# Performance work log

Hardware: AMD Instinct MI355X
Metric: run time of the kernel (lower is better)

Reference implementation:

```python
import jax, jax.numpy as jnp
import numpy as np

T, B, D, H, DEPTH = 256, 64, 1024, 1024, 2


def setup_inputs() -> dict:
    key = jax.random.key(0)
    ks = jax.random.split(key, 12)
    s_in = (1.0 / (D + H)) ** 0.5  # torch Linear default init scale
    s_h = (1.0 / H) ** 0.5
    qc_v = jax.random.uniform(ks[9], (DEPTH, H, H), jnp.float32, -s_h, s_h)
    # weight_norm init: g = ||v|| per output row, so initial w == v
    qc_g = jnp.linalg.norm(qc_v, axis=2)
    return {
        "inputs": jax.random.normal(ks[0], (T, B, D), jnp.float32),
        "Wf": jax.random.uniform(ks[1], (H, D + H), jnp.float32, -s_in, s_in),
        "bf": jax.random.uniform(ks[2], (H,), jnp.float32, -s_in, s_in),
        "Wi": jax.random.uniform(ks[3], (H, D + H), jnp.float32, -s_in, s_in),
        "bi": jax.random.uniform(ks[4], (H,), jnp.float32, -s_in, s_in),
        "Wu": jax.random.uniform(ks[5], (H, D + H), jnp.float32, -s_in, s_in),
        "bu": jax.random.uniform(ks[6], (H,), jnp.float32, -s_in, s_in),
        "Wo": jax.random.uniform(ks[7], (H, D + H), jnp.float32, -s_in, s_in),
        "bo": jax.random.uniform(ks[8], (H,), jnp.float32, -s_in, s_in),
        "qc_v": qc_v,
        "qc_g": qc_g,
        "qc_b": jax.random.uniform(ks[10], (DEPTH, H), jnp.float32, -s_h, s_h),
    }


def reference(inputs, Wf, bf, Wi, bi, Wu, bu, Wo, bo, qc_v, qc_g, qc_b):
    # weight_norm (dim=0): w = g * v / ||v||_row
    qc_w = qc_g[:, :, None] * qc_v / jnp.linalg.norm(qc_v, axis=2, keepdims=True)

    def qc(x):  # x: [4, B, H] -> tanh(linear) applied DEPTH times (shared across gates)
        for d in range(DEPTH):
            x = jnp.tanh(jnp.einsum('gbh,oh->gbo', x, qc_w[d]) + qc_b[d])
        return x

    h0 = jnp.zeros((inputs.shape[1], bf.shape[0]), inputs.dtype)

    def step(carry, x):
        hx, cx = carry
        comb = jnp.concatenate([x, hx], axis=1)  # [B, D+H]
        f = jax.nn.sigmoid(comb @ Wf.T + bf)
        i = jax.nn.sigmoid(comb @ Wi.T + bi)
        g = jnp.tanh(comb @ Wu.T + bu)
        o = jax.nn.sigmoid(comb @ Wo.T + bo)
        f, i, g, o = qc(jnp.stack([f, i, g, o]))
        cx = f * cx + i * g
        hx = o * jnp.tanh(cx)
        return (hx, cx), hx

    (hx, cx), outputs = jax.lax.scan(step, (h0, h0), inputs)
    return outputs, hx, cx
```

## Files before the change

kernel.cpp:

```cpp
#include <hip/hip_runtime.h>
#include <cstdint>
#include <cstddef>

typedef float f32x4 __attribute__((ext_vector_type(4)));
typedef __bf16 bf16x8 __attribute__((ext_vector_type(8)));

#define T_STEPS 256
#define HD      1024
#define DHK     2048

__device__ __forceinline__ unsigned short f2bf(float f) {
  union { float f; unsigned u; } v; v.f = f;
  unsigned r = v.u + 0x7fffu + ((v.u >> 16) & 1u);
  return (unsigned short)(r >> 16);
}

__device__ __forceinline__ float fast_sigmoid(float x) {
  return 1.0f / (1.0f + __expf(-x));
}
__device__ __forceinline__ float fast_tanh(float x) {
  float e = __expf(2.0f * x);
  return (e - 1.0f) / (e + 1.0f);
}

__device__ __forceinline__ f32x4 mfma16(bf16x8 a, bf16x8 b, f32x4 c) {
  return __builtin_amdgcn_mfma_f32_16x16x32_bf16(a, b, c, 0, 0, 0);
}

#define LOADC(dst, vofs, base, IMM)                                            \
  asm volatile("global_load_dwordx4 %0, %1, %2 offset:" IMM " sc0 sc1"         \
               : "=v"(dst) : "v"(vofs), "s"(base) : "memory")

#define L8(st, vofs, base)                                                     \
  LOADC(st[0], vofs, base, "0");   LOADC(st[1], vofs, base, "64");             \
  LOADC(st[2], vofs, base, "128"); LOADC(st[3], vofs, base, "192");            \
  LOADC(st[4], vofs, base, "256"); LOADC(st[5], vofs, base, "320");            \
  LOADC(st[6], vofs, base, "384"); LOADC(st[7], vofs, base, "448")

#define WAITV0()                                                               \
  do { asm volatile("s_waitcnt vmcnt(0)" ::: "memory");                        \
       __builtin_amdgcn_sched_barrier(0); } while (0)

#define MF8(st, w, accv)                                                       \
  accv = mfma16(st[0], (w)[0], accv); accv = mfma16(st[1], (w)[1], accv);      \
  accv = mfma16(st[2], (w)[2], accv); accv = mfma16(st[3], (w)[3], accv);      \
  accv = mfma16(st[4], (w)[4], accv); accv = mfma16(st[5], (w)[5], accv);      \
  accv = mfma16(st[6], (w)[6], accv); accv = mfma16(st[7], (w)[7], accv)

__device__ __forceinline__ void storec8(void* p, ushort4 v) {
  asm volatile("global_store_dwordx2 %0, %1, off sc0 sc1"
               :: "v"(p), "v"(v) : "memory");
}
__device__ __forceinline__ void storec2(void* p, unsigned short v) {
  unsigned vv = v;
  asm volatile("global_store_short %0, %1, off sc0 sc1"
               :: "v"(p), "v"(vv) : "memory");
}

__device__ __forceinline__ void release_flag(int* f, int v) {
  asm volatile("s_waitcnt vmcnt(0)" ::: "memory");
  __hip_atomic_store(f, v, __ATOMIC_RELAXED, __HIP_MEMORY_SCOPE_AGENT);
}
__device__ __forceinline__ void wait_ge(const int* f, int v) {
  while (__hip_atomic_load(f, __ATOMIC_RELAXED, __HIP_MEMORY_SCOPE_AGENT) < v)
    __builtin_amdgcn_s_sleep(2);
  asm volatile("" ::: "memory");
}

__global__ __launch_bounds__(256, 1) void qlstm_persist(
    const unsigned short* __restrict__ Xbf,
    const unsigned short* __restrict__ Wbf,
    const unsigned short* __restrict__ qcw,
    const float* __restrict__ bias_cat,
    const float* __restrict__ qcb,
    unsigned short* __restrict__ Gbf,
    unsigned short* __restrict__ G2bf,
    unsigned short* __restrict__ hbf,
    float* __restrict__ c_state,
    float* __restrict__ out,
    int* __restrict__ aA, int* __restrict__ aB, int* __restrict__ aC) {
  const int nb = blockIdx.x, tid = threadIdx.x;
  const int wv = tid >> 6, lane = tid & 63;
  const int l15 = lane & 15, l16 = lane >> 4;
  const int q = nb >> 6;
  const int n0 = (nb & 63) * 16;
  const int kb = wv * 256;

  __shared__ __align__(16) float red[4][16][68];

  bf16x8 wA[16], wB[8], wC[8];
  {
    const unsigned short* wrow = Wbf + (size_t)(nb * 16 + l15) * DHK;
#pragma unroll
    for (int s = 0; s < 8; ++s)
      wA[s] = *(const bf16x8*)&wrow[kb + s * 32 + l16 * 8];
#pragma unroll
    for (int s = 0; s < 8; ++s)
      wA[8 + s] = *(const bf16x8*)&wrow[1024 + kb + s * 32 + l16 * 8];
    const unsigned short* qrow0 = qcw + (size_t)(n0 + l15) * HD;
    const unsigned short* qrow1 = qrow0 + (size_t)HD * HD;
#pragma unroll
    for (int s = 0; s < 8; ++s) {
      wB[s] = *(const bf16x8*)&qrow0[kb + s * 32 + l16 * 8];
      wC[s] = *(const bf16x8*)&qrow1[kb + s * 32 + l16 * 8];
    }
  }
  const f32x4 biasA = *(const f32x4*)&bias_cat[nb * 16 + (tid & 3) * 4];
  const f32x4 biasB = *(const f32x4*)&qcb[n0 + (tid & 3) * 4];
  const float biasC = qcb[HD + n0 + (tid & 15)];

  const int erow = tid >> 2, ecb = (tid & 3) * 4;
  const int bl = tid >> 4, cc = tid & 15;

  int vofsAB[4], vofsC[4];
#pragma unroll
  for (int mt = 0; mt < 4; ++mt) {
    vofsAB[mt] = (((mt * 16 + l15) * HD) + kb + l16 * 8) * 2;
    vofsC[mt]  = (((mt * 64 + q * 16 + l15) * HD) + kb + l16 * 8) * 2;
  }
  const unsigned short* hB  = hbf;
  const unsigned short* gB  = Gbf + (size_t)(q * 64) * HD;
  const unsigned short* g2B = G2bf;

  for (int t = 0; t < T_STEPS; ++t) {
    {
      f32x4 acc[4] = {};
      const unsigned short* xb = Xbf + (size_t)t * (64 * HD);
#pragma unroll
      for (int s = 0; s < 8; ++s) {
        const int k = kb + s * 32 + l16 * 8;
#pragma unroll
        for (int mt = 0; mt < 4; ++mt) {
          bf16x8 a = *(const bf16x8*)&xb[(size_t)(mt * 16 + l15) * HD + k];
          acc[mt] = mfma16(a, wA[s], acc[mt]);
        }
      }
      wait_ge(&aC[tid], t);
      __syncthreads();
      {
        bf16x8 s0[8], s1[8], s2[8], s3[8];
        L8(s0, vofsAB[0], hB); L8(s1, vofsAB[1], hB);
        L8(s2, vofsAB[2], hB); L8(s3, vofsAB[3], hB);
        WAITV0();
        MF8(s0, wA + 8, acc[0]); MF8(s1, wA + 8, acc[1]);
        MF8(s2, wA + 8, acc[2]); MF8(s3, wA + 8, acc[3]);
      }
#pragma unroll
      for (int mt = 0; mt < 4; ++mt)
        *(f32x4*)&red[wv][l15][mt * 16 + l16 * 4] = acc[mt];
      __syncthreads();
      ushort4 pk;
#pragma unroll
      for (int i = 0; i < 4; ++i) {
        float v = red[0][ecb + i][erow] + red[1][ecb + i][erow] +
                  red[2][ecb + i][erow] + red[3][ecb + i][erow] + biasA[i];
        v = (q == 2) ? fast_tanh(v) : fast_sigmoid(v);
        ((unsigned short*)&pk)[i] = f2bf(v);
      }
      storec8(&Gbf[(size_t)(q * 64 + erow) * HD + n0 + ecb], pk);
      __syncthreads();
      if (tid == 0) release_flag(&aA[nb], t + 1);
    }
    {
      if (tid < 64) wait_ge(&aA[q * 64 + tid], t + 1);
      __syncthreads();
      f32x4 acc[4] = {};
      {
        bf16x8 s0[8], s1[8], s2[8], s3[8];
        L8(s0, vofsAB[0], gB); L8(s1, vofsAB[1], gB);
        L8(s2, vofsAB[2], gB); L8(s3, vofsAB[3], gB);
        WAITV0();
        MF8(s0, wB, acc[0]); MF8(s1, wB, acc[1]);
        MF8(s2, wB, acc[2]); MF8(s3, wB, acc[3]);
      }
#pragma unroll
      for (int mt = 0; mt < 4; ++mt)
        *(f32x4*)&red[wv][l15][mt * 16 + l16 * 4] = acc[mt];
      __syncthreads();
      ushort4 pk;
#pragma unroll
      for (int i = 0; i < 4; ++i) {
        float v = red[0][ecb + i][erow] + red[1][ecb + i][erow] +
                  red[2][ecb + i][erow] + red[3][ecb + i][erow] + biasB[i];
        ((unsigned short*)&pk)[i] = f2bf(fast_tanh(v));
      }
      storec8(&G2bf[(size_t)(q * 64 + erow) * HD + n0 + ecb], pk);
      __syncthreads();
      if (tid == 0) release_flag(&aB[nb], t + 1);
    }
    {
      wait_ge(&aB[tid], t + 1);
      __syncthreads();
      f32x4 acc[4] = {};
      {
        bf16x8 s0[8], s1[8], s2[8], s3[8];
        L8(s0, vofsC[0], g2B); L8(s1, vofsC[1], g2B);
        L8(s2, vofsC[2], g2B); L8(s3, vofsC[3], g2B);
        WAITV0();
        MF8(s0, wC, acc[0]); MF8(s1, wC, acc[1]);
        MF8(s2, wC, acc[2]); MF8(s3, wC, acc[3]);
      }
#pragma unroll
      for (int mt = 0; mt < 4; ++mt)
        *(f32x4*)&red[wv][l15][mt * 16 + l16 * 4] = acc[mt];
      __syncthreads();
      float gv[4];
#pragma unroll
      for (int g = 0; g < 4; ++g) {
        float v = red[0][cc][g * 16 + bl] + red[1][cc][g * 16 + bl] +
                  red[2][cc][g * 16 + bl] + red[3][cc][g * 16 + bl] + biasC;
        gv[g] = fast_tanh(v);
      }
      const int ci = (q * 16 + bl) * HD + n0 + cc;
      const float c_new = gv[0] * c_state[ci] + gv[1] * gv[2];
      const float h_new = gv[3] * fast_tanh(c_new);
      c_state[ci] = c_new;
      out[(size_t)t * (64 * HD) + ci] = h_new;
      storec2(&hbf[ci], f2bf(h_new));
      if (t == T_STEPS - 1) {
        out[(size_t)T_STEPS * (64 * HD) + ci] = h_new;
        out[(size_t)T_STEPS * (64 * HD) + 64 * HD + ci] = c_new;
      }
      __syncthreads();
      if (tid == 0) release_flag(&aC[nb], t + 1);
    }
  }
}

__global__ void xconv_kernel(const float* __restrict__ x,
                             unsigned short* __restrict__ xbf, int n4) {
  int idx = blockIdx.x * blockDim.x + threadIdx.x;
  int stride = gridDim.x * blockDim.x;
  for (int i = idx; i < n4; i += stride) {
    float4 v = ((const float4*)x)[i];
    ushort4 o;
    o.x = f2bf(v.x); o.y = f2bf(v.y); o.z = f2bf(v.z); o.w = f2bf(v.w);
    ((ushort4*)xbf)[i] = o;
  }
}

__global__ void wconv_kernel(const float* __restrict__ Wf, const float* __restrict__ Wi,
                             const float* __restrict__ Wu, const float* __restrict__ Wo,
                             const float* __restrict__ bfv, const float* __restrict__ biv,
                             const float* __restrict__ buv, const float* __restrict__ bov,
                             unsigned short* __restrict__ Wbf, float* __restrict__ bias_cat) {
  const int n = blockIdx.x;
  const int gate = n >> 10, r = n & 1023;
  const float* W = gate == 0 ? Wf : gate == 1 ? Wi : gate == 2 ? Wu : Wo;
  const float* src = W + (size_t)r * DHK;
  unsigned short* dst = Wbf + (size_t)n * DHK;
  for (int k = threadIdx.x; k < DHK; k += 256) dst[k] = f2bf(src[k]);
  if (threadIdx.x == 0) {
    const float* bsrc = gate == 0 ? bfv : gate == 1 ? biv : gate == 2 ? buv : bov;
    bias_cat[n] = bsrc[r];
  }
}

__global__ void qcw_kernel(const float* __restrict__ qcv, const float* __restrict__ qcg,
                           unsigned short* __restrict__ qcw) {
  const int row = blockIdx.x * 4 + (threadIdx.x >> 6);
  const int lane = threadIdx.x & 63;
  const float* v = qcv + (size_t)row * HD;
  float ss = 0.0f;
#pragma unroll
  for (int j = 0; j < 16; ++j) { float a = v[j * 64 + lane]; ss += a * a; }
#pragma unroll
  for (int off = 32; off > 0; off >>= 1) ss += __shfl_xor(ss, off);
  const float scale = qcg[row] / sqrtf(ss);
#pragma unroll
  for (int j = 0; j < 16; ++j)
    qcw[(size_t)row * HD + j * 64 + lane] = f2bf(v[j * 64 + lane] * scale);
}

__global__ void init_state_kernel(unsigned short* __restrict__ hbf,
                                  float* __restrict__ c_state,
                                  int* __restrict__ flags) {
  int i = blockIdx.x * blockDim.x + threadIdx.x;
  hbf[i] = 0;
  c_state[i] = 0.0f;
  if (i < 768) flags[i] = 0;
}

extern "C" void kernel_launch(void* const* d_in, const int* in_sizes, int n_in,
                              void* d_out, int out_size, void* d_ws, size_t ws_size,
                              hipStream_t stream) {
  const float* x   = (const float*)d_in[0];
  const float* Wf  = (const float*)d_in[1];
  const float* bfv = (const float*)d_in[2];
  const float* Wi  = (const float*)d_in[3];
  const float* biv = (const float*)d_in[4];
  const float* Wu  = (const float*)d_in[5];
  const float* buv = (const float*)d_in[6];
  const float* Wo  = (const float*)d_in[7];
  const float* bov = (const float*)d_in[8];
  const float* qcv = (const float*)d_in[9];
  const float* qcg = (const float*)d_in[10];
  const float* qcb = (const float*)d_in[11];
  float* out = (float*)d_out;

  char* p = (char*)d_ws;
  auto alloc = [&](size_t bytes) {
    char* r = p; p += (bytes + 255) & ~(size_t)255; return r;
  };
  unsigned short* Xbf  = (unsigned short*)alloc((size_t)T_STEPS * 64 * HD * 2);
  unsigned short* Wbf  = (unsigned short*)alloc((size_t)4096 * DHK * 2);
  unsigned short* qcw  = (unsigned short*)alloc((size_t)2 * HD * HD * 2);
  float* bias_cat      = (float*)alloc((size_t)4096 * 4);
  unsigned short* Gbf  = (unsigned short*)alloc((size_t)256 * HD * 2);
  unsigned short* G2bf = (unsigned short*)alloc((size_t)256 * HD * 2);
  unsigned short* hbf  = (unsigned short*)alloc((size_t)64 * HD * 2);
  float* c_state       = (float*)alloc((size_t)64 * HD * 4);
  int* flags           = (int*)alloc(768 * 4);

  init_state_kernel<<<256, 256, 0, stream>>>(hbf, c_state, flags);
  xconv_kernel<<<2048, 256, 0, stream>>>(x, Xbf, T_STEPS * 64 * HD / 4);
  wconv_kernel<<<4096, 256, 0, stream>>>(Wf, Wi, Wu, Wo, bfv, biv, buv, bov,
                                         Wbf, bias_cat);
  qcw_kernel<<<512, 256, 0, stream>>>(qcv, qcg, qcw);

  qlstm_persist<<<256, 256, 0, stream>>>(
      Xbf, Wbf, qcw, bias_cat, qcb, Gbf, G2bf, hbf, c_state, out,
      flags, flags + 256, flags + 512);
}
```

Before: 6.415 ms.

## Halve persistent grid to 128 blocks with 32 output columns and streamed weights

The persistent LSTM kernel now runs on 128 blocks instead of 256. Each block computes 32 output columns, issuing two MFMA accumulator sets per A tile. Weights are no longer held in registers; they are read from global memory (likely cached) inside each stage. Stores widen to dwordx4 and dword, and fewer flags are polled, which cuts cross-block synchronisation cost. The trade-off is half the CUs sitting idle and weight loads added to every timestep.

```diff
diff --git a/kernel.cpp b/kernel.cpp
--- a/kernel.cpp
+++ b/kernel.cpp
@@ -4,6 +4,7 @@
 
 typedef float f32x4 __attribute__((ext_vector_type(4)));
 typedef __bf16 bf16x8 __attribute__((ext_vector_type(8)));
+typedef unsigned int u32x4 __attribute__((ext_vector_type(4)));
 
 #define T_STEPS 256
 #define HD      1024
@@ -41,20 +42,13 @@
   do { asm volatile("s_waitcnt vmcnt(0)" ::: "memory");                        \
        __builtin_amdgcn_sched_barrier(0); } while (0)
 
-#define MF8(st, w, accv)                                                       \
-  accv = mfma16(st[0], (w)[0], accv); accv = mfma16(st[1], (w)[1], accv);      \
-  accv = mfma16(st[2], (w)[2], accv); accv = mfma16(st[3], (w)[3], accv);      \
-  accv = mfma16(st[4], (w)[4], accv); accv = mfma16(st[5], (w)[5], accv);      \
-  accv = mfma16(st[6], (w)[6], accv); accv = mfma16(st[7], (w)[7], accv)
-
-__device__ __forceinline__ void storec8(void* p, ushort4 v) {
-  asm volatile("global_store_dwordx2 %0, %1, off sc0 sc1"
+__device__ __forceinline__ void storec16(void* p, u32x4 v) {
+  asm volatile("global_store_dwordx4 %0, %1, off sc0 sc1"
                :: "v"(p), "v"(v) : "memory");
 }
-__device__ __forceinline__ void storec2(void* p, unsigned short v) {
-  unsigned vv = v;
-  asm volatile("global_store_short %0, %1, off sc0 sc1"
-               :: "v"(p), "v"(vv) : "memory");
+__device__ __forceinline__ void storec4(void* p, unsigned v) {
+  asm volatile("global_store_dword %0, %1, off sc0 sc1"
+               :: "v"(p), "v"(v) : "memory");
 }
 
 __device__ __forceinline__ void release_flag(int* f, int v) {
@@ -82,144 +76,189 @@
   const int nb = blockIdx.x, tid = threadIdx.x;
   const int wv = tid >> 6, lane = tid & 63;
   const int l15 = lane & 15, l16 = lane >> 4;
-  const int q = nb >> 6;
-  const int n0 = (nb & 63) * 16;
+  const int l16o = l16 * 8;
+  const int q = nb >> 5;
+  const int nsub = (nb & 31) * 32;
   const int kb = wv * 256;
 
-  __shared__ __align__(16) float red[4][16][68];
-
-  bf16x8 wA[16], wB[8], wC[8];
-  {
-    const unsigned short* wrow = Wbf + (size_t)(nb * 16 + l15) * DHK;
-#pragma unroll
-    for (int s = 0; s < 8; ++s)
-      wA[s] = *(const bf16x8*)&wrow[kb + s * 32 + l16 * 8];
-#pragma unroll
-    for (int s = 0; s < 8; ++s)
-      wA[8 + s] = *(const bf16x8*)&wrow[1024 + kb + s * 32 + l16 * 8];
-    const unsigned short* qrow0 = qcw + (size_t)(n0 + l15) * HD;
-    const unsigned short* qrow1 = qrow0 + (size_t)HD * HD;
-#pragma unroll
-    for (int s = 0; s < 8; ++s) {
-      wB[s] = *(const bf16x8*)&qrow0[kb + s * 32 + l16 * 8];
-      wC[s] = *(const bf16x8*)&qrow1[kb + s * 32 + l16 * 8];
-    }
-  }
-  const f32x4 biasA = *(const f32x4*)&bias_cat[nb * 16 + (tid & 3) * 4];
-  const f32x4 biasB = *(const f32x4*)&qcb[n0 + (tid & 3) * 4];
-  const float biasC = qcb[HD + n0 + (tid & 15)];
-
-  const int erow = tid >> 2, ecb = (tid & 3) * 4;
-  const int bl = tid >> 4, cc = tid & 15;
+  __shared__ __align__(16) float red[4][32][68];
+
+  const unsigned short* wA0 = Wbf + (size_t)(nb * 32 + l15) * DHK + kb;
+  const unsigned short* wA1 = wA0 + (size_t)16 * DHK;
+  const unsigned short* wB0 = qcw + (size_t)(nsub + l15) * HD + kb;
+  const unsigned short* wB1 = wB0 + (size_t)16 * HD;
+  const unsigned short* wC0 = wB0 + (size_t)HD * HD;
+  const unsigned short* wC1 = wB1 + (size_t)HD * HD;
 
   int vofsAB[4], vofsC[4];
 #pragma unroll
   for (int mt = 0; mt < 4; ++mt) {
-    vofsAB[mt] = (((mt * 16 + l15) * HD) + kb + l16 * 8) * 2;
-    vofsC[mt]  = (((mt * 64 + q * 16 + l15) * HD) + kb + l16 * 8) * 2;
-  }
-  const unsigned short* hB  = hbf;
-  const unsigned short* gB  = Gbf + (size_t)(q * 64) * HD;
-  const unsigned short* g2B = G2bf;
+    vofsAB[mt] = ((mt * 16 + l15) * HD + kb + l16o) * 2;
+    vofsC[mt]  = ((mt * 64 + q * 16 + l15) * HD + kb + l16o) * 2;
+  }
+
+  const int erow = tid >> 2, ecb = (tid & 3) * 8;
+  const int bl = tid >> 4, cl = (tid & 15) * 2;
+  float bA[8], bB[8];
+#pragma unroll
+  for (int i = 0; i < 8; ++i) {
+    bA[i] = bias_cat[nb * 32 + ecb + i];
+    bB[i] = qcb[nsub + ecb + i];
+  }
+  const float bC0 = qcb[HD + nsub + cl], bC1 = qcb[HD + nsub + cl + 1];
+
+  const unsigned short* hB = hbf;
+  const unsigned short* gB = Gbf + (size_t)(q * 64) * HD;
 
   for (int t = 0; t < T_STEPS; ++t) {
     {
-      f32x4 acc[4] = {};
+      f32x4 acc[4][2] = {};
       const unsigned short* xb = Xbf + (size_t)t * (64 * HD);
 #pragma unroll
       for (int s = 0; s < 8; ++s) {
-        const int k = kb + s * 32 + l16 * 8;
+        bf16x8 w0 = *(const bf16x8*)&wA0[s * 32 + l16o];
+        bf16x8 w1 = *(const bf16x8*)&wA1[s * 32 + l16o];
 #pragma unroll
         for (int mt = 0; mt < 4; ++mt) {
-          bf16x8 a = *(const bf16x8*)&xb[(size_t)(mt * 16 + l15) * HD + k];
-          acc[mt] = mfma16(a, wA[s], acc[mt]);
+          bf16x8 a =
+              *(const bf16x8*)&xb[(size_t)(mt * 16 + l15) * HD + kb + s * 32 + l16o];
+          acc[mt][0] = mfma16(a, w0, acc[mt][0]);
+          acc[mt][1] = mfma16(a, w1, acc[mt][1]);
         }
       }
-      wait_ge(&aC[tid], t);
+      if (tid < 128) wait_ge(&aC[tid], t);
       __syncthreads();
       {
-        bf16x8 s0[8], s1[8], s2[8], s3[8];
-        L8(s0, vofsAB[0], hB); L8(s1, vofsAB[1], hB);
-        L8(s2, vofsAB[2], hB); L8(s3, vofsAB[3], hB);
+        bf16x8 st0[8], st1[8], st2[8], st3[8];
+        L8(st0, vofsAB[0], hB); L8(st1, vofsAB[1], hB);
+        L8(st2, vofsAB[2], hB); L8(st3, vofsAB[3], hB);
         WAITV0();
-        MF8(s0, wA + 8, acc[0]); MF8(s1, wA + 8, acc[1]);
-        MF8(s2, wA + 8, acc[2]); MF8(s3, wA + 8, acc[3]);
+#pragma unroll
+        for (int s = 0; s < 8; ++s) {
+          bf16x8 w0 = *(const bf16x8*)&wA0[1024 + s * 32 + l16o];
+          bf16x8 w1 = *(const bf16x8*)&wA1[1024 + s * 32 + l16o];
+          acc[0][0] = mfma16(st0[s], w0, acc[0][0]);
+          acc[0][1] = mfma16(st0[s], w1, acc[0][1]);
+          acc[1][0] = mfma16(st1[s], w0, acc[1][0]);
+          acc[1][1] = mfma16(st1[s], w1, acc[1][1]);
+          acc[2][0] = mfma16(st2[s], w0, acc[2][0]);
+          acc[2][1] = mfma16(st2[s], w1, acc[2][1]);
+          acc[3][0] = mfma16(st3[s], w0, acc[3][0]);
+          acc[3][1] = mfma16(st3[s], w1, acc[3][1]);
+        }
       }
 #pragma unroll
       for (int mt = 0; mt < 4; ++mt)
-        *(f32x4*)&red[wv][l15][mt * 16 + l16 * 4] = acc[mt];
-      __syncthreads();
-      ushort4 pk;
-#pragma unroll
-      for (int i = 0; i < 4; ++i) {
-        float v = red[0][ecb + i][erow] + red[1][ecb + i][erow] +
-                  red[2][ecb + i][erow] + red[3][ecb + i][erow] + biasA[i];
+#pragma unroll
+        for (int g = 0; g < 2; ++g)
+          *(f32x4*)&red[wv][g * 16 + l15][mt * 16 + l16 * 4] = acc[mt][g];
+      __syncthreads();
+      union { u32x4 u4; unsigned short us[8]; } pk;
+#pragma unroll
+      for (int i = 0; i < 8; ++i) {
+        const int c = ecb + i;
+        float v = red[0][c][erow] + red[1][c][erow] +
+                  red[2][c][erow] + red[3][c][erow] + bA[i];
         v = (q == 2) ? fast_tanh(v) : fast_sigmoid(v);
-        ((unsigned short*)&pk)[i] = f2bf(v);
-      }
-      storec8(&Gbf[(size_t)(q * 64 + erow) * HD + n0 + ecb], pk);
+        pk.us[i] = f2bf(v);
+      }
+      storec16(&Gbf[(size_t)(q * 64 + erow) * HD + nsub + ecb], pk.u4);
       __syncthreads();
       if (tid == 0) release_flag(&aA[nb], t + 1);
     }
     {
-      if (tid < 64) wait_ge(&aA[q * 64 + tid], t + 1);
-      __syncthreads();
-      f32x4 acc[4] = {};
+      if (tid < 32) wait_ge(&aA[q * 32 + tid], t + 1);
+      __syncthreads();
+      f32x4 acc[4][2] = {};
       {
-        bf16x8 s0[8], s1[8], s2[8], s3[8];
-        L8(s0, vofsAB[0], gB); L8(s1, vofsAB[1], gB);
-        L8(s2, vofsAB[2], gB); L8(s3, vofsAB[3], gB);
+        bf16x8 st0[8], st1[8], st2[8], st3[8];
+        L8(st0, vofsAB[0], gB); L8(st1, vofsAB[1], gB);
+        L8(st2, vofsAB[2], gB); L8(st3, vofsAB[3], gB);
         WAITV0();
-        MF8(s0, wB, acc[0]); MF8(s1, wB, acc[1]);
-        MF8(s2, wB, acc[2]); MF8(s3, wB, acc[3]);
+#pragma unroll
+        for (int s = 0; s < 8; ++s) {
+          bf16x8 w0 = *(const bf16x8*)&wB0[s * 32 + l16o];
+          bf16x8 w1 = *(const bf16x8*)&wB1[s * 32 + l16o];
+          acc[0][0] = mfma16(st0[s], w0, acc[0][0]);
+          acc[0][1] = mfma16(st0[s], w1, acc[0][1]);
+          acc[1][0] = mfma16(st1[s], w0, acc[1][0]);
+          acc[1][1] = mfma16(st1[s], w1, acc[1][1]);
+          acc[2][0] = mfma16(st2[s], w0, acc[2][0]);
+          acc[2][1] = mfma16(st2[s], w1, acc[2][1]);
+          acc[3][0] = mfma16(st3[s], w0, acc[3][0]);
+          acc[3][1] = mfma16(st3[s], w1, acc[3][1]);
+        }
       }
 #pragma unroll
       for (int mt = 0; mt < 4; ++mt)
-        *(f32x4*)&red[wv][l15][mt * 16 + l16 * 4] = acc[mt];
-      __syncthreads();
-      ushort4 pk;
-#pragma unroll
-      for (int i = 0; i < 4; ++i) {
-        float v = red[0][ecb + i][erow] + red[1][ecb + i][erow] +
-                  red[2][ecb + i][erow] + red[3][ecb + i][erow] + biasB[i];
-        ((unsigned short*)&pk)[i] = f2bf(fast_tanh(v));
-      }
-      storec8(&G2bf[(size_t)(q * 64 + erow) * HD + n0 + ecb], pk);
+#pragma unroll
+        for (int g = 0; g < 2; ++g)
+          *(f32x4*)&red[wv][g * 16 + l15][mt * 16 + l16 * 4] = acc[mt][g];
+      __syncthreads();
+      union { u32x4 u4; unsigned short us[8]; } pk;
+#pragma unroll
+      for (int i = 0; i < 8; ++i) {
+        const int c = ecb + i;
+        float v = red[0][c][erow] + red[1][c][erow] +
+                  red[2][c][erow] + red[3][c][erow] + bB[i];
+        pk.us[i] = f2bf(fast_tanh(v));
+      }
+      storec16(&G2bf[(size_t)(q * 64 + erow) * HD + nsub + ecb], pk.u4);
       __syncthreads();
       if (tid == 0) release_flag(&aB[nb], t + 1);
     }
     {
-      wait_ge(&aB[tid], t + 1);
-      __syncthreads();
-      f32x4 acc[4] = {};
+      if (tid < 128) wait_ge(&aB[tid], t + 1);
+      __syncthreads();
+      f32x4 acc[4][2] = {};
       {
-        bf16x8 s0[8], s1[8], s2[8], s3[8];
-        L8(s0, vofsC[0], g2B); L8(s1, vofsC[1], g2B);
-        L8(s2, vofsC[2], g2B); L8(s3, vofsC[3], g2B);
+        bf16x8 st0[8], st1[8], st2[8], st3[8];
+        L8(st0, vofsC[0], G2bf); L8(st1, vofsC[1], G2bf);
+        L8(st2, vofsC[2], G2bf); L8(st3, vofsC[3], G2bf);
         WAITV0();
-        MF8(s0, wC, acc[0]); MF8(s1, wC, acc[1]);
-        MF8(s2, wC, acc[2]); MF8(s3, wC, acc[3]);
+#pragma unroll
+        for (int s = 0; s < 8; ++s) {
+          bf16x8 w0 = *(const bf16x8*)&wC0[s * 32 + l16o];
+          bf16x8 w1 = *(const bf16x8*)&wC1[s * 32 + l16o];
+          acc[0][0] = mfma16(st0[s], w0, acc[0][0]);
+          acc[0][1] = mfma16(st0[s], w1, acc[0][1]);
+          acc[1][0] = mfma16(st1[s], w0, acc[1][0]);
+          acc[1][1] = mfma16(st1[s], w1, acc[1][1]);
+          acc[2][0] = mfma16(st2[s], w0, acc[2][0]);
+          acc[2][1] = mfma16(st2[s], w1, acc[2][1]);
+          acc[3][0] = mfma16(st3[s], w0, acc[3][0]);
+          acc[3][1] = mfma16(st3[s], w1, acc[3][1]);
+        }
       }
 #pragma unroll
       for (int mt = 0; mt < 4; ++mt)
-        *(f32x4*)&red[wv][l15][mt * 16 + l16 * 4] = acc[mt];
-      __syncthreads();
-      float gv[4];
-#pragma unroll
-      for (int g = 0; g < 4; ++g) {
-        float v = red[0][cc][g * 16 + bl] + red[1][cc][g * 16 + bl] +
-                  red[2][cc][g * 16 + bl] + red[3][cc][g * 16 + bl] + biasC;
-        gv[g] = fast_tanh(v);
-      }
-      const int ci = (q * 16 + bl) * HD + n0 + cc;
-      const float c_new = gv[0] * c_state[ci] + gv[1] * gv[2];
-      const float h_new = gv[3] * fast_tanh(c_new);
-      c_state[ci] = c_new;
-      out[(size_t)t * (64 * HD) + ci] = h_new;
-      storec2(&hbf[ci], f2bf(h_new));
+#pragma unroll
+        for (int g = 0; g < 2; ++g)
+          *(f32x4*)&red[wv][g * 16 + l15][mt * 16 + l16 * 4] = acc[mt][g];
+      __syncthreads();
+      float gv0[4], gv1[4];
+#pragma unroll
+      for (int g4 = 0; g4 < 4; ++g4) {
+        float v0 = red[0][cl][g4 * 16 + bl] + red[1][cl][g4 * 16 + bl] +
+                   red[2][cl][g4 * 16 + bl] + red[3][cl][g4 * 16 + bl] + bC0;
+        float v1 = red[0][cl + 1][g4 * 16 + bl] + red[1][cl + 1][g4 * 16 + bl] +
+                   red[2][cl + 1][g4 * 16 + bl] + red[3][cl + 1][g4 * 16 + bl] + bC1;
+        gv0[g4] = fast_tanh(v0);
+        gv1[g4] = fast_tanh(v1);
+      }
+      const int ci = (q * 16 + bl) * HD + nsub + cl;
+      const float cn0 = gv0[0] * c_state[ci] + gv0[1] * gv0[2];
+      const float cn1 = gv1[0] * c_state[ci + 1] + gv1[1] * gv1[2];
+      const float hn0 = gv0[3] * fast_tanh(cn0);
+      const float hn1 = gv1[3] * fast_tanh(cn1);
+      c_state[ci] = cn0; c_state[ci + 1] = cn1;
+      *(float2*)&out[(size_t)t * (64 * HD) + ci] = make_float2(hn0, hn1);
+      unsigned hp = (unsigned)f2bf(hn0) | ((unsigned)f2bf(hn1) << 16);
+      storec4(&hbf[ci], hp);
       if (t == T_STEPS - 1) {
-        out[(size_t)T_STEPS * (64 * HD) + ci] = h_new;
-        out[(size_t)T_STEPS * (64 * HD) + 64 * HD + ci] = c_new;
+        *(float2*)&out[(size_t)T_STEPS * (64 * HD) + ci] = make_float2(hn0, hn1);
+        *(float2*)&out[(size_t)T_STEPS * (64 * HD) + 64 * HD + ci] =
+            make_float2(cn0, cn1);
       }
       __syncthreads();
       if (tid == 0) release_flag(&aC[nb], t + 1);
@@ -278,7 +317,7 @@
   int i = blockIdx.x * blockDim.x + threadIdx.x;
   hbf[i] = 0;
   c_state[i] = 0.0f;
-  if (i < 768) flags[i] = 0;
+  if (i < 384) flags[i] = 0;
 }
 
 extern "C" void kernel_launch(void* const* d_in, const int* in_sizes, int n_in,
@@ -310,7 +349,7 @@
   unsigned short* G2bf = (unsigned short*)alloc((size_t)256 * HD * 2);
   unsigned short* hbf  = (unsigned short*)alloc((size_t)64 * HD * 2);
   float* c_state       = (float*)alloc((size_t)64 * HD * 4);
-  int* flags           = (int*)alloc(768 * 4);
+  int* flags           = (int*)alloc(384 * 4);
 
   init_state_kernel<<<256, 256, 0, stream>>>(hbf, c_state, flags);
   xconv_kernel<<<2048, 256, 0, stream>>>(x, Xbf, T_STEPS * 64 * HD / 4);
@@ -318,7 +357,7 @@
                                          Wbf, bias_cat);
   qcw_kernel<<<512, 256, 0, stream>>>(qcv, qcg, qcw);
 
-  qlstm_persist<<<256, 256, 0, stream>>>(
+  qlstm_persist<<<128, 256, 0, stream>>>(
       Xbf, Wbf, qcw, bias_cat, qcb, Gbf, G2bf, hbf, c_state, out,
-      flags, flags + 256, flags + 512);
-}
+      flags, flags + 128, flags + 256);
+}
```

After: 8.123 ms. 1.27x slower.

## Split work by batch rows per wave, keep weights in LDS, use per-wave epoch flags

Applied to the files above, without the earlier changes.

Each wave now computes a full-K dot product for its own 16 batch rows instead of a K-slice, which removes the LDS cross-wave reduction and the block-wide barriers. Weights move from registers into 128 KB of dynamic LDS. The block-level flags are replaced by per-wave epoch counters that consumers poll with vector loads, so each wave waits only on the rows it needs. Cell state stays in a register rather than global memory. In exchange there are more flag stores and polls, 2-byte scattered stores, and LDS reads of the weights on every step.

```diff
diff --git a/kernel.cpp b/kernel.cpp
--- a/kernel.cpp
+++ b/kernel.cpp
@@ -4,17 +4,18 @@
 
 typedef float f32x4 __attribute__((ext_vector_type(4)));
 typedef __bf16 bf16x8 __attribute__((ext_vector_type(8)));
+typedef unsigned int u32x4 __attribute__((ext_vector_type(4)));
 
 #define T_STEPS 256
 #define HD      1024
 #define DHK     2048
+#define LDSW_BYTES (128 * 64 * 16)
 
 __device__ __forceinline__ unsigned short f2bf(float f) {
   union { float f; unsigned u; } v; v.f = f;
   unsigned r = v.u + 0x7fffu + ((v.u >> 16) & 1u);
   return (unsigned short)(r >> 16);
 }
-
 __device__ __forceinline__ float fast_sigmoid(float x) {
   return 1.0f / (1.0f + __expf(-x));
 }
@@ -22,49 +23,70 @@
   float e = __expf(2.0f * x);
   return (e - 1.0f) / (e + 1.0f);
 }
-
 __device__ __forceinline__ f32x4 mfma16(bf16x8 a, bf16x8 b, f32x4 c) {
   return __builtin_amdgcn_mfma_f32_16x16x32_bf16(a, b, c, 0, 0, 0);
 }
 
-#define LOADC(dst, vofs, base, IMM)                                            \
+#define LOADB(dst, vofs, base, IMM)                                            \
   asm volatile("global_load_dwordx4 %0, %1, %2 offset:" IMM " sc0 sc1"         \
                : "=v"(dst) : "v"(vofs), "s"(base) : "memory")
 
-#define L8(st, vofs, base)                                                     \
-  LOADC(st[0], vofs, base, "0");   LOADC(st[1], vofs, base, "64");             \
-  LOADC(st[2], vofs, base, "128"); LOADC(st[3], vofs, base, "192");            \
-  LOADC(st[4], vofs, base, "256"); LOADC(st[5], vofs, base, "320");            \
-  LOADC(st[6], vofs, base, "384"); LOADC(st[7], vofs, base, "448")
+#define L32(d, vofs, base)                                                     \
+  LOADB(d[0],vofs,base,"0");    LOADB(d[1],vofs,base,"64");                    \
+  LOADB(d[2],vofs,base,"128");  LOADB(d[3],vofs,base,"192");                   \
+  LOADB(d[4],vofs,base,"256");  LOADB(d[5],vofs,base,"320");                   \
+  LOADB(d[6],vofs,base,"384");  LOADB(d[7],vofs,base,"448");                   \
+  LOADB(d[8],vofs,base,"512");  LOADB(d[9],vofs,base,"576");                   \
+  LOADB(d[10],vofs,base,"640"); LOADB(d[11],vofs,base,"704");                  \
+  LOADB(d[12],vofs,base,"768"); LOADB(d[13],vofs,base,"832");                  \
+  LOADB(d[14],vofs,base,"896"); LOADB(d[15],vofs,base,"960");                  \
+  LOADB(d[16],vofs,base,"1024");LOADB(d[17],vofs,base,"1088");                 \
+  LOADB(d[18],vofs,base,"1152");LOADB(d[19],vofs,base,"1216");                 \
+  LOADB(d[20],vofs,base,"1280");LOADB(d[21],vofs,base,"1344");                 \
+  LOADB(d[22],vofs,base,"1408");LOADB(d[23],vofs,base,"1472");                 \
+  LOADB(d[24],vofs,base,"1536");LOADB(d[25],vofs,base,"1600");                 \
+  LOADB(d[26],vofs,base,"1664");LOADB(d[27],vofs,base,"1728");                 \
+  LOADB(d[28],vofs,base,"1792");LOADB(d[29],vofs,base,"1856");                 \
+  LOADB(d[30],vofs,base,"1920");LOADB(d[31],vofs,base,"1984")
 
 #define WAITV0()                                                               \
   do { asm volatile("s_waitcnt vmcnt(0)" ::: "memory");                        \
        __builtin_amdgcn_sched_barrier(0); } while (0)
 
-#define MF8(st, w, accv)                                                       \
-  accv = mfma16(st[0], (w)[0], accv); accv = mfma16(st[1], (w)[1], accv);      \
-  accv = mfma16(st[2], (w)[2], accv); accv = mfma16(st[3], (w)[3], accv);      \
-  accv = mfma16(st[4], (w)[4], accv); accv = mfma16(st[5], (w)[5], accv);      \
-  accv = mfma16(st[6], (w)[6], accv); accv = mfma16(st[7], (w)[7], accv)
-
-__device__ __forceinline__ void storec8(void* p, ushort4 v) {
-  asm volatile("global_store_dwordx2 %0, %1, off sc0 sc1"
-               :: "v"(p), "v"(v) : "memory");
-}
 __device__ __forceinline__ void storec2(void* p, unsigned short v) {
   unsigned vv = v;
   asm volatile("global_store_short %0, %1, off sc0 sc1"
                :: "v"(p), "v"(vv) : "memory");
 }
-
-__device__ __forceinline__ void release_flag(int* f, int v) {
-  asm volatile("s_waitcnt vmcnt(0)" ::: "memory");
-  __hip_atomic_store(f, v, __ATOMIC_RELAXED, __HIP_MEMORY_SCOPE_AGENT);
-}
-__device__ __forceinline__ void wait_ge(const int* f, int v) {
-  while (__hip_atomic_load(f, __ATOMIC_RELAXED, __HIP_MEMORY_SCOPE_AGENT) < v)
-    __builtin_amdgcn_s_sleep(2);
-  asm volatile("" ::: "memory");
+__device__ __forceinline__ void storec4(void* p, unsigned v) {
+  asm volatile("global_store_dword %0, %1, off sc0 sc1"
+               :: "v"(p), "v"(v) : "memory");
+}
+
+__device__ __forceinline__ void poll4(const unsigned* base, int vofs,
+                                      unsigned tgt) {
+  while (true) {
+    u32x4 e;
+    asm volatile("global_load_dwordx4 %0, %1, %2 sc0 sc1"
+                 : "=v"(e) : "v"(vofs), "s"(base) : "memory");
+    asm volatile("s_waitcnt vmcnt(0)" ::: "memory");
+    int ok = (e[0] == tgt) & (e[1] == tgt) & (e[2] == tgt) & (e[3] == tgt);
+    if (__all(ok)) break;
+    __builtin_amdgcn_s_sleep(1);
+  }
+  __builtin_amdgcn_sched_barrier(0);
+}
+__device__ __forceinline__ void poll1(const unsigned* base, int vofs,
+                                      unsigned tgt) {
+  while (true) {
+    unsigned e;
+    asm volatile("global_load_dword %0, %1, %2 sc0 sc1"
+                 : "=v"(e) : "v"(vofs), "s"(base) : "memory");
+    asm volatile("s_waitcnt vmcnt(0)" ::: "memory");
+    if (__all((int)(e == tgt))) break;
+    __builtin_amdgcn_s_sleep(1);
+  }
+  __builtin_amdgcn_sched_barrier(0);
 }
 
 __global__ __launch_bounds__(256, 1) void qlstm_persist(
@@ -76,153 +98,130 @@
     unsigned short* __restrict__ Gbf,
     unsigned short* __restrict__ G2bf,
     unsigned short* __restrict__ hbf,
-    float* __restrict__ c_state,
     float* __restrict__ out,
-    int* __restrict__ aA, int* __restrict__ aB, int* __restrict__ aC) {
+    unsigned* __restrict__ eG, unsigned* __restrict__ eG2,
+    unsigned* __restrict__ eH) {
+  extern __shared__ char lds_raw[];
+  u32x4* lw = (u32x4*)lds_raw;
+
   const int nb = blockIdx.x, tid = threadIdx.x;
   const int wv = tid >> 6, lane = tid & 63;
   const int l15 = lane & 15, l16 = lane >> 4;
-  const int q = nb >> 6;
+  const int l16o = l16 * 8;
+  const int g = nb >> 6;
   const int n0 = (nb & 63) * 16;
-  const int kb = wv * 256;
-
-  __shared__ __align__(16) float red[4][16][68];
-
-  bf16x8 wA[16], wB[8], wC[8];
+  const int n0g = nb & 63;
+
   {
-    const unsigned short* wrow = Wbf + (size_t)(nb * 16 + l15) * DHK;
-#pragma unroll
-    for (int s = 0; s < 8; ++s)
-      wA[s] = *(const bf16x8*)&wrow[kb + s * 32 + l16 * 8];
-#pragma unroll
-    for (int s = 0; s < 8; ++s)
-      wA[8 + s] = *(const bf16x8*)&wrow[1024 + kb + s * 32 + l16 * 8];
-    const unsigned short* qrow0 = qcw + (size_t)(n0 + l15) * HD;
-    const unsigned short* qrow1 = qrow0 + (size_t)HD * HD;
-#pragma unroll
-    for (int s = 0; s < 8; ++s) {
-      wB[s] = *(const bf16x8*)&qrow0[kb + s * 32 + l16 * 8];
-      wC[s] = *(const bf16x8*)&qrow1[kb + s * 32 + l16 * 8];
+    const int ls = tid & 63, j0 = tid >> 6;
+    const int s15 = ls & 15, s16o = (ls >> 4) * 8;
+#pragma unroll
+    for (int jj = 0; jj < 32; ++jj) {
+      const int win = jj * 4 + j0;
+      const unsigned short* src;
+      if (win < 32)
+        src = Wbf + (size_t)(nb * 16 + s15) * DHK + win * 32 + s16o;
+      else if (win < 64)
+        src = Wbf + (size_t)(nb * 16 + s15) * DHK + 1024 + (win - 32) * 32 + s16o;
+      else if (win < 96)
+        src = qcw + (size_t)(n0 + s15) * HD + (win - 64) * 32 + s16o;
+      else
+        src = qcw + (size_t)HD * HD + (size_t)(n0 + s15) * HD + (win - 96) * 32 + s16o;
+      lw[win * 64 + ls] = *(const u32x4*)src;
     }
   }
-  const f32x4 biasA = *(const f32x4*)&bias_cat[nb * 16 + (tid & 3) * 4];
-  const f32x4 biasB = *(const f32x4*)&qcb[n0 + (tid & 3) * 4];
-  const float biasC = qcb[HD + n0 + (tid & 15)];
-
-  const int erow = tid >> 2, ecb = (tid & 3) * 4;
-  const int bl = tid >> 4, cc = tid & 15;
-
-  int vofsAB[4], vofsC[4];
-#pragma unroll
-  for (int mt = 0; mt < 4; ++mt) {
-    vofsAB[mt] = (((mt * 16 + l15) * HD) + kb + l16 * 8) * 2;
-    vofsC[mt]  = (((mt * 64 + q * 16 + l15) * HD) + kb + l16 * 8) * 2;
-  }
-  const unsigned short* hB  = hbf;
-  const unsigned short* gB  = Gbf + (size_t)(q * 64) * HD;
-  const unsigned short* g2B = G2bf;
+  __syncthreads();
+
+  const int vA = ((wv * 16 + l15) * HD + l16o) * 2;
+  const int vB = ((g * 64 + wv * 16 + l15) * HD + l16o) * 2;
+  const int crow = (l15 & 3) * 64 + g * 16 + wv * 4 + (l15 >> 2);
+  const int vC = (crow * HD + l16o) * 2;
+  const int veH = (wv * 256 + lane * 4) * 4;
+  const int veG = ((wv * 4 + g) * 64 + lane) * 4;
+  const int veG2 = (g * 256 + lane * 4) * 4;
+
+  const float bA = bias_cat[nb * 16 + l15];
+  const float bB = qcb[n0 + l15];
+  const float bC = qcb[HD + n0 + l15];
+  const int colA = n0 + l15;
+  const int batchC = g * 16 + wv * 4 + l16;
+
+  float c_reg = 0.0f;
+  bf16x8 d[32];
 
   for (int t = 0; t < T_STEPS; ++t) {
     {
-      f32x4 acc[4] = {};
+      f32x4 a0 = {}, a1 = {};
       const unsigned short* xb = Xbf + (size_t)t * (64 * HD);
 #pragma unroll
-      for (int s = 0; s < 8; ++s) {
-        const int k = kb + s * 32 + l16 * 8;
-#pragma unroll
-        for (int mt = 0; mt < 4; ++mt) {
-          bf16x8 a = *(const bf16x8*)&xb[(size_t)(mt * 16 + l15) * HD + k];
-          acc[mt] = mfma16(a, wA[s], acc[mt]);
-        }
-      }
-      wait_ge(&aC[tid], t);
-      __syncthreads();
-      {
-        bf16x8 s0[8], s1[8], s2[8], s3[8];
-        L8(s0, vofsAB[0], hB); L8(s1, vofsAB[1], hB);
-        L8(s2, vofsAB[2], hB); L8(s3, vofsAB[3], hB);
-        WAITV0();
-        MF8(s0, wA + 8, acc[0]); MF8(s1, wA + 8, acc[1]);
-        MF8(s2, wA + 8, acc[2]); MF8(s3, wA + 8, acc[3]);
-      }
-#pragma unroll
-      for (int mt = 0; mt < 4; ++mt)
-        *(f32x4*)&red[wv][l15][mt * 16 + l16 * 4] = acc[mt];
-      __syncthreads();
-      ushort4 pk;
+      for (int w = 0; w < 32; w += 2) {
+        bf16x8 x0 = *(const bf16x8*)&xb[(size_t)(wv * 16 + l15) * HD + w * 32 + l16o];
+        bf16x8 x1 = *(const bf16x8*)&xb[(size_t)(wv * 16 + l15) * HD + (w + 1) * 32 + l16o];
+        a0 = mfma16(x0, *(const bf16x8*)&lw[w * 64 + lane], a0);
+        a1 = mfma16(x1, *(const bf16x8*)&lw[(w + 1) * 64 + lane], a1);
+      }
+      poll4(eH, veH, (unsigned)t);
+      L32(d, vA, hbf);
+      WAITV0();
+#pragma unroll
+      for (int w = 0; w < 32; w += 2) {
+        a0 = mfma16(d[w],     *(const bf16x8*)&lw[(32 + w) * 64 + lane], a0);
+        a1 = mfma16(d[w + 1], *(const bf16x8*)&lw[(33 + w) * 64 + lane], a1);
+      }
+      f32x4 acc = a0 + a1;
 #pragma unroll
       for (int i = 0; i < 4; ++i) {
-        float v = red[0][ecb + i][erow] + red[1][ecb + i][erow] +
-                  red[2][ecb + i][erow] + red[3][ecb + i][erow] + biasA[i];
-        v = (q == 2) ? fast_tanh(v) : fast_sigmoid(v);
-        ((unsigned short*)&pk)[i] = f2bf(v);
-      }
-      storec8(&Gbf[(size_t)(q * 64 + erow) * HD + n0 + ecb], pk);
-      __syncthreads();
-      if (tid == 0) release_flag(&aA[nb], t + 1);
+        const int row = g * 64 + wv * 16 + l16 * 4 + i;
+        float v = acc[i] + bA;
+        v = (g == 2) ? fast_tanh(v) : fast_sigmoid(v);
+        storec2(&Gbf[(size_t)row * HD + colA], f2bf(v));
+      }
+      asm volatile("s_waitcnt vmcnt(0)" ::: "memory");
+      if (lane == 0) storec4(&eG[(wv * 4 + g) * 64 + n0g], (unsigned)(t + 1));
     }
     {
-      if (tid < 64) wait_ge(&aA[q * 64 + tid], t + 1);
-      __syncthreads();
-      f32x4 acc[4] = {};
-      {
-        bf16x8 s0[8], s1[8], s2[8], s3[8];
-        L8(s0, vofsAB[0], gB); L8(s1, vofsAB[1], gB);
-        L8(s2, vofsAB[2], gB); L8(s3, vofsAB[3], gB);
-        WAITV0();
-        MF8(s0, wB, acc[0]); MF8(s1, wB, acc[1]);
-        MF8(s2, wB, acc[2]); MF8(s3, wB, acc[3]);
-      }
-#pragma unroll
-      for (int mt = 0; mt < 4; ++mt)
-        *(f32x4*)&red[wv][l15][mt * 16 + l16 * 4] = acc[mt];
-      __syncthreads();
-      ushort4 pk;
+      poll1(eG, veG, (unsigned)(t + 1));
+      L32(d, vB, Gbf);
+      WAITV0();
+      f32x4 a0 = {}, a1 = {};
+#pragma unroll
+      for (int w = 0; w < 32; w += 2) {
+        a0 = mfma16(d[w],     *(const bf16x8*)&lw[(64 + w) * 64 + lane], a0);
+        a1 = mfma16(d[w + 1], *(const bf16x8*)&lw[(65 + w) * 64 + lane], a1);
+      }
+      f32x4 acc = a0 + a1;
 #pragma unroll
       for (int i = 0; i < 4; ++i) {
-        float v = red[0][ecb + i][erow] + red[1][ecb + i][erow] +
-                  red[2][ecb + i][erow] + red[3][ecb + i][erow] + biasB[i];
-        ((unsigned short*)&pk)[i] = f2bf(fast_tanh(v));
-      }
-      storec8(&G2bf[(size_t)(q * 64 + erow) * HD + n0 + ecb], pk);
-      __syncthreads();
-      if (tid == 0) release_flag(&aB[nb], t + 1);
+        const int row = g * 64 + wv * 16 + l16 * 4 + i;
+        storec2(&G2bf[(size_t)row * HD + colA], f2bf(fast_tanh(acc[i] + bB)));
+      }
+      asm volatile("s_waitcnt vmcnt(0)" ::: "memory");
+      if (lane == 0) storec4(&eG2[(wv * 4 + g) * 64 + n0g], (unsigned)(t + 1));
     }
     {
-      wait_ge(&aB[tid], t + 1);
-      __syncthreads();
-      f32x4 acc[4] = {};
-      {
-        bf16x8 s0[8], s1[8], s2[8], s3[8];
-        L8(s0, vofsC[0], g2B); L8(s1, vofsC[1], g2B);
-        L8(s2, vofsC[2], g2B); L8(s3, vofsC[3], g2B);
-        WAITV0();
-        MF8(s0, wC, acc[0]); MF8(s1, wC, acc[1]);
-        MF8(s2, wC, acc[2]); MF8(s3, wC, acc[3]);
-      }
-#pragma unroll
-      for (int mt = 0; mt < 4; ++mt)
-        *(f32x4*)&red[wv][l15][mt * 16 + l16 * 4] = acc[mt];
-      __syncthreads();
+      poll4(eG2, veG2, (unsigned)(t + 1));
+      L32(d, vC, G2bf);
+      WAITV0();
+      f32x4 a0 = {}, a1 = {};
+#pragma unroll
+      for (int w = 0; w < 32; w += 2) {
+        a0 = mfma16(d[w],     *(const bf16x8*)&lw[(96 + w) * 64 + lane], a0);
+        a1 = mfma16(d[w + 1], *(const bf16x8*)&lw[(97 + w) * 64 + lane], a1);
+      }
+      f32x4 acc = a0 + a1;
       float gv[4];
 #pragma unroll
-      for (int g = 0; g < 4; ++g) {
-        float v = red[0][cc][g * 16 + bl] + red[1][cc][g * 16 + bl] +
-                  red[2][cc][g * 16 + bl] + red[3][cc][g * 16 + bl] + biasC;
-        gv[g] = fast_tanh(v);
-      }
-      const int ci = (q * 16 + bl) * HD + n0 + cc;
-      const float c_new = gv[0] * c_state[ci] + gv[1] * gv[2];
-      const float h_new = gv[3] * fast_tanh(c_new);
-      c_state[ci] = c_new;
-      out[(size_t)t * (64 * HD) + ci] = h_new;
-      storec2(&hbf[ci], f2bf(h_new));
+      for (int i = 0; i < 4; ++i) gv[i] = fast_tanh(acc[i] + bC);
+      c_reg = gv[0] * c_reg + gv[1] * gv[2];
+      const float h_new = gv[3] * fast_tanh(c_reg);
+      storec2(&hbf[(size_t)batchC * HD + colA], f2bf(h_new));
+      asm volatile("s_waitcnt vmcnt(0)" ::: "memory");
+      if (lane == 0) storec4(&eH[(g * 4 + wv) * 64 + n0g], (unsigned)(t + 1));
+      out[(size_t)t * (64 * HD) + batchC * HD + colA] = h_new;
       if (t == T_STEPS - 1) {
-        out[(size_t)T_STEPS * (64 * HD) + ci] = h_new;
-        out[(size_t)T_STEPS * (64 * HD) + 64 * HD + ci] = c_new;
-      }
-      __syncthreads();
-      if (tid == 0) release_flag(&aC[nb], t + 1);
+        out[(size_t)T_STEPS * (64 * HD) + batchC * HD + colA] = h_new;
+        out[(size_t)T_STEPS * (64 * HD) + 64 * HD + batchC * HD + colA] = c_reg;
+      }
     }
   }
 }
@@ -273,12 +272,10 @@
 }
 
 __global__ void init_state_kernel(unsigned short* __restrict__ hbf,
-                                  float* __restrict__ c_state,
-                                  int* __restrict__ flags) {
+                                  unsigned* __restrict__ epochs) {
   int i = blockIdx.x * blockDim.x + threadIdx.x;
   hbf[i] = 0;
-  c_state[i] = 0.0f;
-  if (i < 768) flags[i] = 0;
+  if (i < 3072) epochs[i] = 0;
 }
 
 extern "C" void kernel_launch(void* const* d_in, const int* in_sizes, int n_in,
@@ -309,16 +306,22 @@
   unsigned short* Gbf  = (unsigned short*)alloc((size_t)256 * HD * 2);
   unsigned short* G2bf = (unsigned short*)alloc((size_t)256 * HD * 2);
   unsigned short* hbf  = (unsigned short*)alloc((size_t)64 * HD * 2);
-  float* c_state       = (float*)alloc((size_t)64 * HD * 4);
-  int* flags           = (int*)alloc(768 * 4);
-
-  init_state_kernel<<<256, 256, 0, stream>>>(hbf, c_state, flags);
+  unsigned* epochs     = (unsigned*)alloc(3072 * 4);
+
+  static int lds_set = 0;
+  if (!lds_set) {
+    hipFuncSetAttribute((const void*)qlstm_persist,
+                        hipFuncAttributeMaxDynamicSharedMemorySize, LDSW_BYTES);
+    lds_set = 1;
+  }
+
+  init_state_kernel<<<256, 256, 0, stream>>>(hbf, epochs);
   xconv_kernel<<<2048, 256, 0, stream>>>(x, Xbf, T_STEPS * 64 * HD / 4);
   wconv_kernel<<<4096, 256, 0, stream>>>(Wf, Wi, Wu, Wo, bfv, biv, buv, bov,
                                          Wbf, bias_cat);
   qcw_kernel<<<512, 256, 0, stream>>>(qcv, qcg, qcw);
 
-  qlstm_persist<<<256, 256, 0, stream>>>(
-      Xbf, Wbf, qcw, bias_cat, qcb, Gbf, G2bf, hbf, c_state, out,
-      flags, flags + 256, flags + 512);
-}
+  qlstm_persist<<<256, 256, LDSW_BYTES, stream>>>(
+      Xbf, Wbf, qcw, bias_cat, qcb, Gbf, G2bf, hbf, out,
+      epochs, epochs + 1024, epochs + 2048);
+}
```

Result: slower. 9.055 ms (+41.1%).
